# Kernel optimization log

Measured on AMD Instinct MI355X. Metric: run time of the kernel, lower is better.

## Reference

```python
import jax, jax.numpy as jnp
import numpy as np
from jax import lax

IMG = 512            # image H = W
FH = FW = 32         # feature map spatial size
A = 9                # anchors per location (3 sizes x 3 ratios)
N = FH * FW * A      # total anchors = 9216
IOU_THR = 0.7
MIN_SCORE = 0.5
MIN_SIZE = 1e-3


def make_anchors():
    """Anchors in centroid format (cx, cy, w, h), ordered (H, W, A)."""
    stride = IMG / FH
    sizes = np.array([32.0, 64.0, 128.0])
    ratios = np.array([0.5, 1.0, 2.0])
    ws = (sizes[:, None] / np.sqrt(ratios)[None, :]).reshape(-1)  # (A,)
    hs = (sizes[:, None] * np.sqrt(ratios)[None, :]).reshape(-1)  # (A,)
    cx = (np.arange(FW) + 0.5) * stride
    cy = (np.arange(FH) + 0.5) * stride
    CX = np.broadcast_to(cx[None, :, None], (FH, FW, A))
    CY = np.broadcast_to(cy[:, None, None], (FH, FW, A))
    Wg = np.broadcast_to(ws[None, None, :], (FH, FW, A))
    Hg = np.broadcast_to(hs[None, None, :], (FH, FW, A))
    anc = np.stack([CX, CY, Wg, Hg], axis=-1).reshape(-1, 4)
    return jnp.asarray(anc, dtype=jnp.float32)


def pairwise_iou(b):
    # b: (N,4) corners x1,y1,x2,y2
    x1, y1, x2, y2 = b[:, 0], b[:, 1], b[:, 2], b[:, 3]
    area = (x2 - x1) * (y2 - y1)
    ix1 = jnp.maximum(x1[:, None], x1[None, :])
    iy1 = jnp.maximum(y1[:, None], y1[None, :])
    ix2 = jnp.minimum(x2[:, None], x2[None, :])
    iy2 = jnp.minimum(y2[:, None], y2[None, :])
    inter = jnp.maximum(ix2 - ix1, 0.0) * jnp.maximum(iy2 - iy1, 0.0)
    union = area[:, None] + area[None, :] - inter
    return inter / jnp.maximum(union, 1e-9)


def nms_keep(boxes, scores, valid):
    """Greedy NMS. Returns bool keep mask of shape (N,). Index decisions only."""
    s = jnp.where(valid, scores, -jnp.inf)
    order = jnp.argsort(-s)
    b = boxes[order]
    v = valid[order]
    ious = pairwise_iou(b)  # (N, N)
    idx = jnp.arange(N)

    def body(i, supp):
        keep_i = (~supp[i]) & v[i]
        return supp | (keep_i & (ious[i] > IOU_THR) & (idx > i))

    supp = lax.fori_loop(0, N, body, jnp.zeros(N, dtype=bool))
    keep_sorted = (~supp) & v
    return jnp.zeros(N, dtype=bool).at[order].set(keep_sorted)


def setup_inputs() -> dict:
    key = jax.random.key(0)
    ks = jax.random.split(key, 4)
    return {
        "feature_map": jax.random.normal(ks[0], (1, 256, FH, FW), jnp.float32),
        "conv1_w": jax.random.normal(ks[1], (512, 256, 3, 3), jnp.float32) * 0.02,
        "conv1_b": jnp.zeros((512,), jnp.float32),
        "conv2_w": jax.random.normal(ks[2], (A, 512), jnp.float32) * 0.01,
        "conv2_b": jnp.zeros((A,), jnp.float32),
        "conv3_w": jax.random.normal(ks[3], (4 * A, 512), jnp.float32) * 0.01,
        "conv3_b": jnp.zeros((4 * A,), jnp.float32),
    }


def reference(feature_map, conv1_w, conv1_b, conv2_w, conv2_b, conv3_w, conv3_b):
    anchors = make_anchors()  # (N,4) cx,cy,w,h

    # --- conv backbone head ---
    h = lax.conv_general_dilated(
        feature_map, conv1_w, (1, 1), "SAME",
        dimension_numbers=("NCHW", "OIHW", "NCHW"))
    h = jax.nn.relu(h + conv1_b[None, :, None, None])  # (1,512,H,W)

    scores = jax.nn.sigmoid(
        jnp.einsum("bchw,ac->bahw", h, conv2_w) + conv2_b[None, :, None, None])
    scores = scores.transpose(0, 2, 3, 1).reshape(-1)  # (N,) ordered (H,W,A)

    off = jnp.einsum("bchw,oc->bohw", h, conv3_w) + conv3_b[None, :, None, None]
    off = off.reshape(1, A, 4, FH, FW).transpose(0, 3, 4, 1, 2).reshape(-1, 4)

    acx, acy, aw, ah = anchors[:, 0], anchors[:, 1], anchors[:, 2], anchors[:, 3]
    cx = acx + off[:, 0] * aw
    cy = acy + off[:, 1] * ah
    bw = aw * jnp.exp(off[:, 2])
    bh = ah * jnp.exp(off[:, 3])
    boxes = jnp.stack([cx - bw / 2, cy - bh / 2, cx + bw / 2, cy + bh / 2], axis=1)

    # --- clip to image ---
    lo = jnp.array([0.0, 0.0, 0.0, 0.0], jnp.float32)
    hi = jnp.array([IMG, IMG, IMG, IMG], jnp.float32)
    boxes = jnp.clip(boxes, lo, hi)

    # --- remove small boxes + score threshold (as a mask, jit-safe) ---
    valid = ((boxes[:, 2] - boxes[:, 0]) >= MIN_SIZE) \
          & ((boxes[:, 3] - boxes[:, 1]) >= MIN_SIZE) \
          & (scores >= MIN_SCORE)

    # --- NMS (selection is index-based; no gradient through the decision) ---
    keep = nms_keep(lax.stop_gradient(boxes), lax.stop_gradient(scores), valid)

    out = jnp.concatenate(
        [boxes * keep[:, None].astype(boxes.dtype),
         (scores * keep.astype(scores.dtype))[:, None]], axis=1)  # (N,5)
    return out
```

## Files before the change

### kernel.cpp

```cpp
#include <hip/hip_runtime.h>
#include <math.h>

#define FHW   32
#define NA    9
#define NBOX  9216
#define C1    256
#define C2    512
#define KTOT  2304
#define KS    8
#define KCH   (KTOT / KS)
#define CAP   64

struct AnchorWH { float w[NA]; float h[NA]; };

#define FP_OFF    0u
#define WT_OFF    1183744u
#define HP_OFF    5902336u
#define BOX_OFF   22679552u
#define SC_OFF    22827008u
#define VL_OFF    22863872u
#define DEG_OFF   22900736u
#define ADJ_OFF   22937600u
#define NV_OFF    24117248u

__global__ __launch_bounds__(256) void k_prep(const float* __restrict__ fin,
                                              float* __restrict__ Fp,
                                              unsigned int* __restrict__ deg,
                                              unsigned int* __restrict__ nv,
                                              const float* __restrict__ w1,
                                              float* __restrict__ Wt) {
    if (blockIdx.x < 1156) {
        int idx = blockIdx.x * 256 + threadIdx.x;
        if (idx < 256 * 34 * 34) {
            int c   = idx / 1156;
            int rem = idx - c * 1156;
            int yy  = rem / 34;
            int xx  = rem - yy * 34;
            float v = 0.f;
            if (yy >= 1 && yy <= 32 && xx >= 1 && xx <= 32)
                v = fin[c * 1024 + (yy - 1) * 32 + (xx - 1)];
            Fp[idx] = v;
        }
        if (idx < NBOX) deg[idx] = 0u;
        if (idx == 0)   *nv = 0u;
    } else {
        __shared__ float tile[32][33];
        int tb  = blockIdx.x - 1156;
        int k0  = (tb % 72) * 32;
        int oc0 = (tb / 72) * 32;
        int t   = threadIdx.x;
        int r0 = t >> 5, c = t & 31;
        #pragma unroll
        for (int i = 0; i < 4; ++i) {
            int r = r0 + 8 * i;
            tile[r][c] = w1[(oc0 + r) * KTOT + k0 + c];
        }
        __syncthreads();
        #pragma unroll
        for (int i = 0; i < 4; ++i) {
            int kk = r0 + 8 * i;
            Wt[(k0 + kk) * C2 + oc0 + c] = tile[c][kk];
        }
    }
}

__global__ __launch_bounds__(256, 2) void k_gemm(const float* __restrict__ Fp,
                                                 const float* __restrict__ Wt,
                                                 float* __restrict__ hp) {
    const int id = blockIdx.x;
    const int bx = id >> 5, g = id & 31;
    const int by = g >> 3, kz = g & 7;
    const int p0  = bx * 64;
    const int oc0 = by * 128;
    const int k0b = kz * KCH;
    const int t  = threadIdx.x;
    const int ty = t >> 4, tx = t & 15;

    __shared__ float As[16][64];
    __shared__ float Bs[16][128];

    float acc[4][8];
    #pragma unroll
    for (int r = 0; r < 4; ++r)
        #pragma unroll
        for (int c = 0; c < 8; ++c) acc[r][c] = 0.f;

    for (int kt = 0; kt < KCH; kt += 16) {
        #pragma unroll
        for (int i = 0; i < 4; ++i) {
            int e  = t + 256 * i;
            int kk = e >> 6, pp = e & 63;
            int k   = k0b + kt + kk;
            int c   = k / 9;
            int kap = k - c * 9;
            int dy  = kap / 3;
            int dx  = kap - dy * 3;
            int p  = p0 + pp;
            int y  = p >> 5, x = p & 31;
            As[kk][pp] = Fp[(c * 34 + y + dy) * 34 + x + dx];
        }
        #pragma unroll
        for (int i = 0; i < 2; ++i) {
            int e4 = t + 256 * i;
            int kk = e4 >> 5, c4 = e4 & 31;
            *(float4*)&Bs[kk][c4 * 4] =
                *(const float4*)&Wt[(k0b + kt + kk) * C2 + oc0 + c4 * 4];
        }
        __syncthreads();
        #pragma unroll
        for (int kk = 0; kk < 16; ++kk) {
            float a[4], b[8];
            *(float4*)&a[0] = *(const float4*)&As[kk][ty * 4];
            *(float4*)&b[0] = *(const float4*)&Bs[kk][tx * 4];
            *(float4*)&b[4] = *(const float4*)&Bs[kk][tx * 4 + 64];
            #pragma unroll
            for (int r = 0; r < 4; ++r)
                #pragma unroll
                for (int c = 0; c < 8; ++c) acc[r][c] += a[r] * b[c];
        }
        __syncthreads();
    }
    #pragma unroll
    for (int r = 0; r < 4; ++r) {
        int p = p0 + ty * 4 + r;
        float* dst = hp + ((kz * 1024 + p) * C2 + oc0 + tx * 4);
        *(float4*)dst        = *(float4*)&acc[r][0];
        *(float4*)(dst + 64) = *(float4*)&acc[r][4];
    }
}

__global__ __launch_bounds__(256) void k_heads(const float* __restrict__ hp,
                                               const float* __restrict__ b1,
                                               const float* __restrict__ w2,
                                               const float* __restrict__ b2,
                                               const float* __restrict__ w3,
                                               const float* __restrict__ b3,
                                               float* __restrict__ boxes,
                                               float* __restrict__ scoresG,
                                               unsigned int* __restrict__ nv,
                                               unsigned int* __restrict__ vlist,
                                               AnchorWH awh) {
    const int p = blockIdx.x;
    const int t = threadIdx.x;
    __shared__ float hrow[C2];
    __shared__ float arr[45];

    #pragma unroll
    for (int i = 0; i < 2; ++i) {
        int c = t + 256 * i;
        float s = b1[c];
        #pragma unroll
        for (int ks = 0; ks < KS; ++ks) s += hp[(ks * 1024 + p) * C2 + c];
        hrow[c] = fmaxf(s, 0.f);
    }
    __syncthreads();

    const int w = t >> 6, lane = t & 63;
    float h8[8];
    #pragma unroll
    for (int i = 0; i < 8; ++i) h8[i] = hrow[lane + 64 * i];

    for (int j = w; j < 45; j += 4) {
        const float* wp = (j < 9) ? (w2 + j * C2) : (w3 + (j - 9) * C2);
        float s = 0.f;
        #pragma unroll
        for (int i = 0; i < 8; ++i) s += h8[i] * wp[lane + 64 * i];
        #pragma unroll
        for (int d = 1; d < 64; d <<= 1) s += __shfl_xor(s, d, 64);
        if (lane == 0) arr[j] = s;
    }
    __syncthreads();

    if (t < NA) {
        int a = t;
        float logit = arr[a] + b2[a];
        float score = 1.f / (1.f + expf(-logit));
        float o0 = arr[9 + a * 4 + 0] + b3[a * 4 + 0];
        float o1 = arr[9 + a * 4 + 1] + b3[a * 4 + 1];
        float o2 = arr[9 + a * 4 + 2] + b3[a * 4 + 2];
        float o3 = arr[9 + a * 4 + 3] + b3[a * 4 + 3];
        int y = p >> 5, x = p & 31;
        float ax = (x + 0.5f) * 16.f, ay = (y + 0.5f) * 16.f;
        float aw = awh.w[a], ah = awh.h[a];
        float cx = ax + o0 * aw;
        float cy = ay + o1 * ah;
        float bw = aw * expf(o2);
        float bh = ah * expf(o3);
        float x1 = fminf(fmaxf(cx - bw * 0.5f, 0.f), 512.f);
        float y1 = fminf(fmaxf(cy - bh * 0.5f, 0.f), 512.f);
        float x2 = fminf(fmaxf(cx + bw * 0.5f, 0.f), 512.f);
        float y2 = fminf(fmaxf(cy + bh * 0.5f, 0.f), 512.f);
        int n = p * 9 + a;
        float4 bx4; bx4.x = x1; bx4.y = y1; bx4.z = x2; bx4.w = y2;
        ((float4*)boxes)[n] = bx4;
        scoresG[n] = score;
        bool valid = (x2 - x1 >= 0.001f) && (y2 - y1 >= 0.001f) && (score >= 0.5f);
        if (valid) {
            unsigned int ci = atomicAdd(nv, 1u);
            vlist[ci] = (unsigned int)n;
        }
    }
}

__global__ __launch_bounds__(256) void k_adj(const unsigned int* __restrict__ nvp,
                                             const unsigned int* __restrict__ vlist,
                                             const float* __restrict__ boxes,
                                             const float* __restrict__ scoresG,
                                             unsigned int* __restrict__ deg,
                                             unsigned short* __restrict__ adj) {
    const int Nv = (int)*nvp;
    int b = blockIdx.x;
    int tv = (int)(sqrtf(2.f * b + 0.25f) - 0.5f);
    while ((tv + 1) * (tv + 2) / 2 <= b) tv++;
    while (tv * (tv + 1) / 2 > b) tv--;
    int tu = b - tv * (tv + 1) / 2;
    if (tv * 128 >= Nv) return;

    __shared__ float4 ub[128], vb[128];
    __shared__ float  us[128], vs[128];
    __shared__ int    uo[128], vo[128];
    int t = threadIdx.x;
    if (t < 128) {
        int gi = tu * 128 + t;
        if (gi < Nv) { int n = (int)vlist[gi]; ub[t] = ((const float4*)boxes)[n]; us[t] = scoresG[n]; uo[t] = n; }
        else us[t] = -1.f;
    } else {
        int tt = t - 128;
        int gj = tv * 128 + tt;
        if (gj < Nv) { int n = (int)vlist[gj]; vb[tt] = ((const float4*)boxes)[n]; vs[tt] = scoresG[n]; vo[tt] = n; }
        else vs[tt] = -1.f;
    }
    __syncthreads();

    for (int s = 0; s < 64; ++s) {
        int q  = t + 256 * s;
        int i  = q >> 7, jj = q & 127;
        if (tu == tv && i >= jj) continue;
        float su = us[i], sv = vs[jj];
        if (su < 0.f || sv < 0.f) continue;
        float4 bu = ub[i], bv = vb[jj];
        float au = (bu.z - bu.x) * (bu.w - bu.y);
        float av = (bv.z - bv.x) * (bv.w - bv.y);
        float ix1 = fmaxf(bu.x, bv.x), iy1 = fmaxf(bu.y, bv.y);
        float ix2 = fminf(bu.z, bv.z), iy2 = fminf(bu.w, bv.w);
        float inter = fmaxf(ix2 - ix1, 0.f) * fmaxf(iy2 - iy1, 0.f);
        float uni = au + av - inter;
        float iou = inter / fmaxf(uni, 1e-9f);
        if (iou > 0.7f) {
            int gi = tu * 128 + i, gj = tv * 128 + jj;
            bool uHigh = (su > sv) || (su == sv && uo[i] < vo[jj]);
            int lower = uHigh ? gj : gi;
            int upper = uHigh ? gi : gj;
            unsigned int slot = atomicAdd(&deg[lower], 1u);
            if (slot < CAP) adj[lower * CAP + slot] = (unsigned short)upper;
        }
    }
}

__global__ __launch_bounds__(512) void k_peel(const unsigned int* __restrict__ nvp,
                                              const unsigned int* __restrict__ vlist,
                                              const unsigned int* __restrict__ deg,
                                              const unsigned short* __restrict__ adj,
                                              const float* __restrict__ boxes,
                                              const float* __restrict__ scoresG,
                                              float* __restrict__ out) {
    __shared__ unsigned char st[NBOX];
    __shared__ unsigned char keepm[NBOX];
    __shared__ int changed;
    const int t = threadIdx.x;
    const int Nv = (int)*nvp;
    for (int n = t; n < NBOX; n += 512) keepm[n] = 0;
    for (int i = t; i < Nv; i += 512) st[i] = 0;
    __syncthreads();

    for (int round = 0; round < 256; ++round) {
        if (t == 0) changed = 0;
        __syncthreads();
        bool any = false;
        for (int i = t; i < Nv; i += 512) {
            if (st[i] == 0) {
                int d = (int)deg[i]; if (d > CAP) d = CAP;
                bool kseen = false, useen = false;
                for (int s = 0; s < d; ++s) {
                    unsigned char v = st[adj[i * CAP + s]];
                    kseen |= (v == 1);
                    useen |= (v == 0);
                }
                if (kseen)      { st[i] = 2; any = true; }
                else if (!useen){ st[i] = 1; any = true; }
            }
        }
        if (any) changed = 1;
        __syncthreads();
        int c = changed;
        __syncthreads();
        if (!c) break;
    }
    for (int i = t; i < Nv; i += 512)
        if (st[i] == 1) keepm[vlist[i]] = 1;
    __syncthreads();

    for (int n = t; n < NBOX; n += 512) {
        float4 b = ((const float4*)boxes)[n];
        bool k = keepm[n] != 0;
        out[n * 5 + 0] = k ? b.x : 0.f;
        out[n * 5 + 1] = k ? b.y : 0.f;
        out[n * 5 + 2] = k ? b.z : 0.f;
        out[n * 5 + 3] = k ? b.w : 0.f;
        out[n * 5 + 4] = k ? scoresG[n] : 0.f;
    }
}

extern "C" void kernel_launch(void* const* d_in, const int* in_sizes, int n_in,
                              void* d_out, int out_size, void* d_ws, size_t ws_size,
                              hipStream_t stream) {
    const float* fin = (const float*)d_in[0];
    const float* w1  = (const float*)d_in[1];
    const float* b1  = (const float*)d_in[2];
    const float* w2  = (const float*)d_in[3];
    const float* b2  = (const float*)d_in[4];
    const float* w3  = (const float*)d_in[5];
    const float* b3  = (const float*)d_in[6];
    float* out = (float*)d_out;

    char* ws = (char*)d_ws;
    float*          Fp    = (float*)(ws + FP_OFF);
    float*          Wt    = (float*)(ws + WT_OFF);
    float*          hp    = (float*)(ws + HP_OFF);
    float*          boxes = (float*)(ws + BOX_OFF);
    float*          sc    = (float*)(ws + SC_OFF);
    unsigned int*   vlist = (unsigned int*)(ws + VL_OFF);
    unsigned int*   deg   = (unsigned int*)(ws + DEG_OFF);
    unsigned short* adj   = (unsigned short*)(ws + ADJ_OFF);
    unsigned int*   nv    = (unsigned int*)(ws + NV_OFF);

    AnchorWH awh;
    {
        const double sizes[3]  = {32.0, 64.0, 128.0};
        const double ratios[3] = {0.5, 1.0, 2.0};
        for (int si = 0; si < 3; ++si)
            for (int ri = 0; ri < 3; ++ri) {
                awh.w[si * 3 + ri] = (float)(sizes[si] / sqrt(ratios[ri]));
                awh.h[si * 3 + ri] = (float)(sizes[si] * sqrt(ratios[ri]));
            }
    }

    k_prep<<<dim3(1156 + 72 * 16), 256, 0, stream>>>(fin, Fp, deg, nv, w1, Wt);
    k_gemm<<<dim3(512), 256, 0, stream>>>(Fp, Wt, hp);
    k_heads<<<dim3(1024), 256, 0, stream>>>(hp, b1, w2, b2, w3, b3, boxes, sc, nv, vlist, awh);
    k_adj<<<dim3(72 * 73 / 2), 256, 0, stream>>>(nv, vlist, boxes, sc, deg, adj);
    k_peel<<<dim3(1), 512, 0, stream>>>(nv, vlist, deg, adj, boxes, sc, out);
}
```

Measured before the change: 209.2 us.

## Stage NMS adjacency as compact CSR in LDS and batch four pixels per heads block

The single-block peel kernel now builds a prefix-summed CSR copy of the adjacency lists in shared memory, with contiguous per-thread vertex ranges, so each iterative round reads neighbours from LDS instead of global memory. Entries that do not fit in the fixed shared capacity fall back to global reads. The final output is written as a zero fill followed by a scatter of only the kept boxes. k_heads now handles four pixels per block, which cuts the grid by four and reuses the weight rows across those pixels, but it gives up the per-thread register cache of the hidden row.

```diff
diff --git a/kernel.cpp b/kernel.cpp
--- a/kernel.cpp
+++ b/kernel.cpp
@@ -10,6 +10,7 @@
 #define KS    8
 #define KCH   (KTOT / KS)
 #define CAP   64
+#define ECAP  12288
 
 struct AnchorWH { float w[NA]; float h[NA]; };
 
@@ -140,45 +141,47 @@
                                                unsigned int* __restrict__ nv,
                                                unsigned int* __restrict__ vlist,
                                                AnchorWH awh) {
-    const int p = blockIdx.x;
-    const int t = threadIdx.x;
-    __shared__ float hrow[C2];
-    __shared__ float arr[45];
+    const int p0 = blockIdx.x * 4;
+    const int t  = threadIdx.x;
+    __shared__ float hrow[4][C2];
+    __shared__ float arr[4][45];
 
     #pragma unroll
-    for (int i = 0; i < 2; ++i) {
-        int c = t + 256 * i;
-        float s = b1[c];
-        #pragma unroll
-        for (int ks = 0; ks < KS; ++ks) s += hp[(ks * 1024 + p) * C2 + c];
-        hrow[c] = fmaxf(s, 0.f);
+    for (int px = 0; px < 4; ++px) {
+        int p = p0 + px;
+        #pragma unroll
+        for (int i = 0; i < 2; ++i) {
+            int c = t + 256 * i;
+            float s = b1[c];
+            #pragma unroll
+            for (int ks = 0; ks < KS; ++ks) s += hp[(ks * 1024 + p) * C2 + c];
+            hrow[px][c] = fmaxf(s, 0.f);
+        }
     }
     __syncthreads();
 
     const int w = t >> 6, lane = t & 63;
-    float h8[8];
-    #pragma unroll
-    for (int i = 0; i < 8; ++i) h8[i] = hrow[lane + 64 * i];
-
-    for (int j = w; j < 45; j += 4) {
+    for (int job = w; job < 180; job += 4) {
+        int px = job / 45, j = job - px * 45;
         const float* wp = (j < 9) ? (w2 + j * C2) : (w3 + (j - 9) * C2);
         float s = 0.f;
         #pragma unroll
-        for (int i = 0; i < 8; ++i) s += h8[i] * wp[lane + 64 * i];
+        for (int i = 0; i < 8; ++i) s += hrow[px][lane + 64 * i] * wp[lane + 64 * i];
         #pragma unroll
         for (int d = 1; d < 64; d <<= 1) s += __shfl_xor(s, d, 64);
-        if (lane == 0) arr[j] = s;
-    }
-    __syncthreads();
-
-    if (t < NA) {
-        int a = t;
-        float logit = arr[a] + b2[a];
+        if (lane == 0) arr[px][j] = s;
+    }
+    __syncthreads();
+
+    if (t < 36) {
+        int px = t / 9, a = t - px * 9;
+        int p = p0 + px;
+        float logit = arr[px][a] + b2[a];
         float score = 1.f / (1.f + expf(-logit));
-        float o0 = arr[9 + a * 4 + 0] + b3[a * 4 + 0];
-        float o1 = arr[9 + a * 4 + 1] + b3[a * 4 + 1];
-        float o2 = arr[9 + a * 4 + 2] + b3[a * 4 + 2];
-        float o3 = arr[9 + a * 4 + 3] + b3[a * 4 + 3];
+        float o0 = arr[px][9 + a * 4 + 0] + b3[a * 4 + 0];
+        float o1 = arr[px][9 + a * 4 + 1] + b3[a * 4 + 1];
+        float o2 = arr[px][9 + a * 4 + 2] + b3[a * 4 + 2];
+        float o3 = arr[px][9 + a * 4 + 3] + b3[a * 4 + 3];
         int y = p >> 5, x = p & 31;
         float ax = (x + 0.5f) * 16.f, ay = (y + 0.5f) * 16.f;
         float aw = awh.w[a], ah = awh.h[a];
@@ -259,35 +262,72 @@
 
 __global__ __launch_bounds__(512) void k_peel(const unsigned int* __restrict__ nvp,
                                               const unsigned int* __restrict__ vlist,
-                                              const unsigned int* __restrict__ deg,
-                                              const unsigned short* __restrict__ adj,
+                                              const unsigned int* __restrict__ degG,
+                                              const unsigned short* __restrict__ adjG,
                                               const float* __restrict__ boxes,
                                               const float* __restrict__ scoresG,
                                               float* __restrict__ out) {
-    __shared__ unsigned char st[NBOX];
-    __shared__ unsigned char keepm[NBOX];
+    __shared__ unsigned char  st[NBOX];
+    __shared__ unsigned char  degL[NBOX];
+    __shared__ unsigned short offL[NBOX];
+    __shared__ unsigned short csr[ECAP];
+    __shared__ unsigned int   scratch[512];
     __shared__ int changed;
-    const int t = threadIdx.x;
+    const int t  = threadIdx.x;
     const int Nv = (int)*nvp;
-    for (int n = t; n < NBOX; n += 512) keepm[n] = 0;
-    for (int i = t; i < Nv; i += 512) st[i] = 0;
+    const int chunk = (Nv + 511) / 512;
+    const int i0 = t * chunk;
+    const int i1 = (i0 + chunk < Nv) ? (i0 + chunk) : Nv;
+
+    unsigned int lsum = 0;
+    for (int i = i0; i < i1; ++i) {
+        unsigned int d = degG[i];
+        if (d > CAP) d = CAP;
+        degL[i] = (unsigned char)d;
+        st[i] = 0;
+        lsum += d;
+    }
+    scratch[t] = lsum;
+    __syncthreads();
+    for (int ofs = 1; ofs < 512; ofs <<= 1) {
+        unsigned int v = (t >= ofs) ? scratch[t - ofs] : 0u;
+        __syncthreads();
+        scratch[t] += v;
+        __syncthreads();
+    }
+    unsigned int base = scratch[t] - lsum;
+    {
+        unsigned int off = base;
+        for (int i = i0; i < i1; ++i) {
+            unsigned int o = (off < ECAP) ? off : ECAP;
+            offL[i] = (unsigned short)o;
+            int d = degL[i];
+            int ld = (int)ECAP - (int)o; if (ld > d) ld = d; if (ld < 0) ld = 0;
+            for (int s = 0; s < ld; ++s)
+                csr[o + s] = adjG[i * CAP + s];
+            off += d;
+        }
+    }
     __syncthreads();
 
     for (int round = 0; round < 256; ++round) {
         if (t == 0) changed = 0;
         __syncthreads();
         bool any = false;
-        for (int i = t; i < Nv; i += 512) {
+        for (int i = i0; i < i1; ++i) {
             if (st[i] == 0) {
-                int d = (int)deg[i]; if (d > CAP) d = CAP;
+                int d   = degL[i];
+                int off = offL[i];
+                int ld  = (int)ECAP - off; if (ld > d) ld = d; if (ld < 0) ld = 0;
                 bool kseen = false, useen = false;
                 for (int s = 0; s < d; ++s) {
-                    unsigned char v = st[adj[i * CAP + s]];
+                    int j = (s < ld) ? (int)csr[off + s] : (int)adjG[i * CAP + s];
+                    unsigned char v = st[j];
                     kseen |= (v == 1);
                     useen |= (v == 0);
                 }
-                if (kseen)      { st[i] = 2; any = true; }
-                else if (!useen){ st[i] = 1; any = true; }
+                if (kseen)       { st[i] = 2; any = true; }
+                else if (!useen) { st[i] = 1; any = true; }
             }
         }
         if (any) changed = 1;
@@ -296,18 +336,22 @@
         __syncthreads();
         if (!c) break;
     }
-    for (int i = t; i < Nv; i += 512)
-        if (st[i] == 1) keepm[vlist[i]] = 1;
-    __syncthreads();
 
     for (int n = t; n < NBOX; n += 512) {
-        float4 b = ((const float4*)boxes)[n];
-        bool k = keepm[n] != 0;
-        out[n * 5 + 0] = k ? b.x : 0.f;
-        out[n * 5 + 1] = k ? b.y : 0.f;
-        out[n * 5 + 2] = k ? b.z : 0.f;
-        out[n * 5 + 3] = k ? b.w : 0.f;
-        out[n * 5 + 4] = k ? scoresG[n] : 0.f;
+        out[n * 5 + 0] = 0.f; out[n * 5 + 1] = 0.f; out[n * 5 + 2] = 0.f;
+        out[n * 5 + 3] = 0.f; out[n * 5 + 4] = 0.f;
+    }
+    __syncthreads();
+    for (int i = t; i < Nv; i += 512) {
+        if (st[i] == 1) {
+            int n = (int)vlist[i];
+            float4 b = ((const float4*)boxes)[n];
+            out[n * 5 + 0] = b.x;
+            out[n * 5 + 1] = b.y;
+            out[n * 5 + 2] = b.z;
+            out[n * 5 + 3] = b.w;
+            out[n * 5 + 4] = scoresG[n];
+        }
     }
 }
 
@@ -347,7 +391,7 @@
 
     k_prep<<<dim3(1156 + 72 * 16), 256, 0, stream>>>(fin, Fp, deg, nv, w1, Wt);
     k_gemm<<<dim3(512), 256, 0, stream>>>(Fp, Wt, hp);
-    k_heads<<<dim3(1024), 256, 0, stream>>>(hp, b1, w2, b2, w3, b3, boxes, sc, nv, vlist, awh);
+    k_heads<<<dim3(256), 256, 0, stream>>>(hp, b1, w2, b2, w3, b3, boxes, sc, nv, vlist, awh);
     k_adj<<<dim3(72 * 73 / 2), 256, 0, stream>>>(nv, vlist, boxes, sc, deg, adj);
     k_peel<<<dim3(1), 512, 0, stream>>>(nv, vlist, deg, adj, boxes, sc, out);
 }
```

Measured after the change: 229.3 us. 1.1x slower.
